# Performance work log

Measured on AMD Instinct MI355X. Metric: run time of the kernel, lower is better.

Reference implementation:

```python
import jax, jax.numpy as jnp
import numpy as np

SIGMA_INIT = 1000.0


def setup_inputs() -> dict:
    key = jax.random.key(0)
    k1, k2, k3 = jax.random.split(key, 3)
    B, M, D, S = 1024, 209, 12288, 2
    input_data = jax.random.normal(k1, (B, D), dtype=jnp.float32)
    center = jax.random.normal(k2, (M, D), dtype=jnp.float32)
    sigma = SIGMA_INIT * jnp.ones((M,), dtype=jnp.float32)
    W = 50.0 * jax.random.normal(k3, (S, M), dtype=jnp.float32)
    b = jnp.zeros((S,), dtype=jnp.float32)
    return {"input_data": input_data, "center": center, "sigma": sigma, "W": W, "b": b}


def reference(input_data, center, sigma, W, b):
    # Euclidean distance ||x_i - c_j|| via GEMM expansion (avoids [B,M,D] diff tensor)
    x2 = jnp.sum(input_data * input_data, axis=1, keepdims=True)        # [B,1]
    c2 = jnp.sum(center * center, axis=1)[None, :]                      # [1,M]
    d2 = x2 + c2 - 2.0 * (input_data @ center.T)                        # [B,M]
    dist = jnp.sqrt(jnp.maximum(d2, 0.0))
    # Note: original divides the (non-squared) norm by sigma^2, then exp(-.)
    radial = jnp.exp(-dist / (sigma * sigma)[None, :])                  # [B,M]
    return radial @ W.T + b                                             # [B,S]
```

## Files before the change

kernel.cpp:

```cpp
#include <hip/hip_runtime.h>
#include <hip/hip_bf16.h>
#include <stdint.h>

#define B_SZ 1024
#define M_SZ 209
#define MPAD 224
#define D_SZ 12288
#define KC   16
#define KCH  768
#define BK   128
#define NIT  (KCH / BK)
#define NB   32
#define BT   32
#define NCT  7
#define SROW 224
#define SLROW (KC * SROW)

#define CBF_OFF  0u
#define XXP_OFF  (MPAD * D_SZ)
#define CCP_OFF  (XXP_OFF + B_SZ * KC * 4)
#define SLAB_OFF (CCP_OFF + MPAD * 2 * 4)

typedef __attribute__((ext_vector_type(8))) short short8;
typedef __attribute__((ext_vector_type(4))) float floatx4;

__device__ __forceinline__ uint32_t pk8x4(const float4& v) {
    int d = __builtin_amdgcn_cvt_pk_fp8_f32(v.x, v.y, 0, false);
    d     = __builtin_amdgcn_cvt_pk_fp8_f32(v.z, v.w, d, true);
    return (uint32_t)d;
}

__device__ __forceinline__ void gload_lds16(const void* g, void* l) {
    __builtin_amdgcn_global_load_lds(
        (const __attribute__((address_space(1))) void*)g,
        (__attribute__((address_space(3))) void*)l, 16, 0, 0);
}

__global__ __launch_bounds__(256) void rbf_prep(
    const float* __restrict__ c, uint8_t* __restrict__ cf8,
    float* __restrict__ ccp)
{
    __shared__ float red[4];
    const int j = blockIdx.x >> 1, h = blockIdx.x & 1;
    const int t = threadIdx.x;
    const int base = h * (D_SZ / 2);
    uint8_t* dst = cf8 + (size_t)j * D_SZ + base;
    float s = 0.f;
    if (j < M_SZ) {
        const float* src = c + (size_t)j * D_SZ + base;
        for (int i = t * 8; i < D_SZ / 2; i += 2048) {
            float4 v0 = *(const float4*)(src + i);
            float4 v1 = *(const float4*)(src + i + 4);
            s += v0.x*v0.x + v0.y*v0.y + v0.z*v0.z + v0.w*v0.w
               + v1.x*v1.x + v1.y*v1.y + v1.z*v1.z + v1.w*v1.w;
            uint2 w = { pk8x4(v0), pk8x4(v1) };
            *(uint2*)(dst + i) = w;
        }
    } else {
        uint2 zz = {0u, 0u};
        for (int i = t * 8; i < D_SZ / 2; i += 2048) *(uint2*)(dst + i) = zz;
    }
#pragma unroll
    for (int off = 32; off > 0; off >>= 1) s += __shfl_down(s, off);
    if ((t & 63) == 0) red[t >> 6] = s;
    __syncthreads();
    if (t == 0) ccp[j * 2 + h] = red[0] + red[1] + red[2] + red[3];
}

__global__ __launch_bounds__(256, 2) void rbf_main(
    const float* __restrict__ x, const uint8_t* __restrict__ cf8,
    uint8_t* __restrict__ slab, float* __restrict__ xxp)
{
    __shared__ uint8_t sx[2][BT * BK];
    __shared__ uint8_t sc[2][MPAD * BK];

    const int t    = threadIdx.x;
    const int k    = blockIdx.x;
    const int b    = blockIdx.y;
    const int wave = t >> 6, lane = t & 63;
    const int quad = lane >> 4, mrow = lane & 15;
    const int qh = quad >> 1, ql = quad & 1;
    const int s2 = (mrow >> 1) & 7;
    const int rt  = wave & 1;
    const int cth = wave >> 1;

    floatx4 acc[NCT];
    const floatx4 z4 = {0.f, 0.f, 0.f, 0.f};
#pragma unroll
    for (int i = 0; i < NCT; ++i) acc[i] = z4;

    const int oE = (((lane & 7) ^ (lane >> 4)) & 7) * 16;
    const int oO = ((((lane & 7) ^ (lane >> 4)) ^ 4) & 7) * 16;
    const uint8_t* cpbE = cf8 + (size_t)(lane >> 3) * D_SZ + (size_t)k * KCH + oE;
    const uint8_t* cpbO = cf8 + (size_t)(lane >> 3) * D_SZ + (size_t)k * KCH + oO;

#pragma unroll
    for (int jj = 0; jj < 7; ++jj) {
        const int cr = wave * 7 + jj;
        const uint8_t* p = ((cr & 1) ? cpbO : cpbE) + (size_t)cr * 8 * D_SZ;
        gload_lds16(p, &sc[0][cr * 1024]);
    }

    const int xr = t >> 3;
    const int xc = t & 7;
    const float* xp = x + (size_t)(b * BT + xr) * D_SZ + (size_t)k * KCH + xc * 16;

    uint4 xw[NIT];
    float sxx = 0.f;
#pragma unroll
    for (int it = 0; it < NIT; ++it) {
        float4 v0 = *(const float4*)(xp + it * BK + 0);
        float4 v1 = *(const float4*)(xp + it * BK + 4);
        float4 v2 = *(const float4*)(xp + it * BK + 8);
        float4 v3 = *(const float4*)(xp + it * BK + 12);
        sxx += v0.x*v0.x + v0.y*v0.y + v0.z*v0.z + v0.w*v0.w
             + v1.x*v1.x + v1.y*v1.y + v1.z*v1.z + v1.w*v1.w
             + v2.x*v2.x + v2.y*v2.y + v2.z*v2.z + v2.w*v2.w
             + v3.x*v3.x + v3.y*v3.y + v3.z*v3.z + v3.w*v3.w;
        xw[it] = make_uint4(pk8x4(v0), pk8x4(v1), pk8x4(v2), pk8x4(v3));
    }
    const int sxoff = xr * BK + ((xc ^ ((xr >> 1) & 7)) & 7) * 16;

    int boff[4];
#pragma unroll
    for (int ks = 0; ks < 4; ++ks)
        boff[ks] = (((ks * 2 + qh) ^ s2) & 7) * 16 + ql * 8;
    const int aoff = (rt * 16 + mrow) * BK;
    const int boff0 = (cth * 7 * 16 + mrow) * BK;

    *(uint4*)&sx[0][sxoff] = xw[0];
    __syncthreads();

#pragma unroll
    for (int it = 0; it < NIT; ++it) {
        const int cur = it & 1;
        if (it + 1 < NIT) {
#pragma unroll
            for (int jj = 0; jj < 7; ++jj) {
                const int cr = wave * 7 + jj;
                const uint8_t* p = ((cr & 1) ? cpbO : cpbE)
                                 + (size_t)cr * 8 * D_SZ + (it + 1) * BK;
                gload_lds16(p, &sc[cur ^ 1][cr * 1024]);
            }
            *(uint4*)&sx[cur ^ 1][sxoff] = xw[it + 1];
        }
#pragma unroll
        for (int ks = 0; ks < 4; ++ks) {
            const long a = *(const long*)(&sx[cur][aoff] + boff[ks]);
#pragma unroll
            for (int ct = 0; ct < NCT; ++ct) {
                const long bv = *(const long*)(&sc[cur][boff0] + ct * 16 * BK + boff[ks]);
                acc[ct] = __builtin_amdgcn_mfma_f32_16x16x32_fp8_fp8(a, bv, acc[ct], 0, 0, 0);
            }
        }
        __syncthreads();
    }

    uint8_t* sd = slab + (size_t)k * SROW;
    const int gi0 = b * BT + rt * 16 + quad * 4;
#pragma unroll
    for (int ct = 0; ct < NCT; ++ct) {
        const int gj = (cth * 7 + ct) * 16 + mrow;
        const int p01 = __builtin_amdgcn_cvt_pk_fp8_f32(acc[ct][0], acc[ct][1], 0, false);
        const int p23 = __builtin_amdgcn_cvt_pk_fp8_f32(acc[ct][2], acc[ct][3], 0, false);
        uint8_t* wb = sd + (size_t)gi0 * SLROW + gj;
        wb[0]                   = (uint8_t)(p01 & 0xff);
        wb[SLROW]               = (uint8_t)((p01 >> 8) & 0xff);
        wb[2 * (size_t)SLROW]   = (uint8_t)(p23 & 0xff);
        wb[3 * (size_t)SLROW]   = (uint8_t)((p23 >> 8) & 0xff);
    }

    sxx += __shfl_down(sxx, 4);
    sxx += __shfl_down(sxx, 2);
    sxx += __shfl_down(sxx, 1);
    if ((t & 7) == 0) xxp[(size_t)(b * BT + xr) * KC + k] = sxx;
}

__global__ __launch_bounds__(256) void rbf_fin(
    const uint8_t* __restrict__ slab, const float* __restrict__ xxp,
    const float* __restrict__ ccp, const float* __restrict__ sigma,
    const float* __restrict__ W, const float* __restrict__ bias,
    float* __restrict__ out)
{
    __shared__ float jpart[MPAD * 9];
    __shared__ float jtot[MPAD];
    __shared__ float xsh;

    const int t = threadIdx.x;
    const int i = blockIdx.x;

    if (t < 64) {
        float xv = (t < KC) ? xxp[(size_t)i * KC + t] : 0.f;
#pragma unroll
        for (int off = 32; off > 0; off >>= 1) xv += __shfl_down(xv, off);
        if (t == 0) xsh = xv;
    }

    const int o = t % 28, g = t / 28;
    if (t < 252) {
        const uint8_t* sp = slab + (size_t)i * SLROW + o * 8;
        float s8[8] = {0.f,0.f,0.f,0.f,0.f,0.f,0.f,0.f};
        for (int kk = g; kk < KC; kk += 9) {
            uint2 v = *(const uint2*)(sp + (size_t)kk * SROW);
            s8[0] += __builtin_amdgcn_cvt_f32_fp8((int)v.x, 0);
            s8[1] += __builtin_amdgcn_cvt_f32_fp8((int)v.x, 1);
            s8[2] += __builtin_amdgcn_cvt_f32_fp8((int)v.x, 2);
            s8[3] += __builtin_amdgcn_cvt_f32_fp8((int)v.x, 3);
            s8[4] += __builtin_amdgcn_cvt_f32_fp8((int)v.y, 0);
            s8[5] += __builtin_amdgcn_cvt_f32_fp8((int)v.y, 1);
            s8[6] += __builtin_amdgcn_cvt_f32_fp8((int)v.y, 2);
            s8[7] += __builtin_amdgcn_cvt_f32_fp8((int)v.y, 3);
        }
#pragma unroll
        for (int e = 0; e < 8; ++e) jpart[(o * 8 + e) * 9 + g] = s8[e];
    }
    __syncthreads();

    if (t < MPAD) {
        float d = 0.f;
#pragma unroll
        for (int g2 = 0; g2 < 9; ++g2) d += jpart[t * 9 + g2];
        jtot[t] = d;
    }
    __syncthreads();

    if (t < 64) {
        const float xxi = xsh;
        float a0 = 0.f, a1 = 0.f;
        for (int j = t; j < M_SZ; j += 64) {
            const float ccj = ccp[j * 2] + ccp[j * 2 + 1];
            float d2 = fmaxf(xxi + ccj - 2.f * jtot[j], 0.f);
            float sg = sigma[j];
            float rad = __expf(-sqrtf(d2) / (sg * sg));
            a0 += rad * W[j];
            a1 += rad * W[M_SZ + j];
        }
#pragma unroll
        for (int off = 32; off > 0; off >>= 1) {
            a0 += __shfl_down(a0, off);
            a1 += __shfl_down(a1, off);
        }
        if (t == 0) {
            out[i * 2 + 0] = a0 + bias[0];
            out[i * 2 + 1] = a1 + bias[1];
        }
    }
}

extern "C" void kernel_launch(void* const* d_in, const int* in_sizes, int n_in,
                              void* d_out, int out_size, void* d_ws, size_t ws_size,
                              hipStream_t stream)
{
    const float* x     = (const float*)d_in[0];
    const float* c     = (const float*)d_in[1];
    const float* sigma = (const float*)d_in[2];
    const float* W     = (const float*)d_in[3];
    const float* bias  = (const float*)d_in[4];
    float* out = (float*)d_out;

    char* ws = (char*)d_ws;
    uint8_t* cf8  = (uint8_t*)(ws + CBF_OFF);
    float*   xxp  = (float*)(ws + XXP_OFF);
    float*   ccp  = (float*)(ws + CCP_OFF);
    uint8_t* slab = (uint8_t*)(ws + SLAB_OFF);

    rbf_prep<<<MPAD * 2, 256, 0, stream>>>(c, cf8, ccp);
    rbf_main<<<dim3(KC, NB), 256, 0, stream>>>(x, cf8, slab, xxp);
    rbf_fin<<<B_SZ, 256, 0, stream>>>(slab, xxp, ccp, sigma, W, bias, out);
}
```

Measured before the change: 110.5 us.

## Fuse finalize kernel into main GEMM via last-block atomic counter

Removes the separate rbf_fin launch. Each main block bumps a per-row-tile atomic counter after writing its fp8 partial slab, and the last of the KC split-K blocks does the reduction, exp and projection for its 32 rows. The counter is reset in the prep kernel. This saves a kernel launch and its gap, but puts the whole epilogue on only 32 blocks, each handling 8 rows per wave serially, which could be slower than the 1024-block finalize.

```diff
diff --git a/kernel.cpp b/kernel.cpp
--- a/kernel.cpp
+++ b/kernel.cpp
@@ -20,8 +20,8 @@
 #define XXP_OFF  (MPAD * D_SZ)
 #define CCP_OFF  (XXP_OFF + B_SZ * KC * 4)
 #define SLAB_OFF (CCP_OFF + MPAD * 2 * 4)
-
-typedef __attribute__((ext_vector_type(8))) short short8;
+#define CNT_OFF  (SLAB_OFF + B_SZ * SLROW)
+
 typedef __attribute__((ext_vector_type(4))) float floatx4;
 
 __device__ __forceinline__ uint32_t pk8x4(const float4& v) {
@@ -38,11 +38,12 @@
 
 __global__ __launch_bounds__(256) void rbf_prep(
     const float* __restrict__ c, uint8_t* __restrict__ cf8,
-    float* __restrict__ ccp)
+    float* __restrict__ ccp, uint32_t* __restrict__ cnt)
 {
     __shared__ float red[4];
     const int j = blockIdx.x >> 1, h = blockIdx.x & 1;
     const int t = threadIdx.x;
+    if (blockIdx.x == 0 && t < NB) cnt[t] = 0u;
     const int base = h * (D_SZ / 2);
     uint8_t* dst = cf8 + (size_t)j * D_SZ + base;
     float s = 0.f;
@@ -69,7 +70,10 @@
 
 __global__ __launch_bounds__(256, 2) void rbf_main(
     const float* __restrict__ x, const uint8_t* __restrict__ cf8,
-    uint8_t* __restrict__ slab, float* __restrict__ xxp)
+    uint8_t* __restrict__ slab, float* __restrict__ xxp,
+    uint32_t* __restrict__ cnt, const float* __restrict__ ccp,
+    const float* __restrict__ sigma, const float* __restrict__ W,
+    const float* __restrict__ bias, float* __restrict__ out)
 {
     __shared__ uint8_t sx[2][BT * BK];
     __shared__ uint8_t sc[2][MPAD * BK];
@@ -125,7 +129,7 @@
 #pragma unroll
     for (int ks = 0; ks < 4; ++ks)
         boff[ks] = (((ks * 2 + qh) ^ s2) & 7) * 16 + ql * 8;
-    const int aoff = (rt * 16 + mrow) * BK;
+    const int aoff  = (rt * 16 + mrow) * BK;
     const int boff0 = (cth * 7 * 16 + mrow) * BK;
 
     *(uint4*)&sx[0][sxoff] = xw[0];
@@ -156,93 +160,82 @@
         __syncthreads();
     }
 
-    uint8_t* sd = slab + (size_t)k * SROW;
-    const int gi0 = b * BT + rt * 16 + quad * 4;
-#pragma unroll
-    for (int ct = 0; ct < NCT; ++ct) {
-        const int gj = (cth * 7 + ct) * 16 + mrow;
-        const int p01 = __builtin_amdgcn_cvt_pk_fp8_f32(acc[ct][0], acc[ct][1], 0, false);
-        const int p23 = __builtin_amdgcn_cvt_pk_fp8_f32(acc[ct][2], acc[ct][3], 0, false);
-        uint8_t* wb = sd + (size_t)gi0 * SLROW + gj;
-        wb[0]                   = (uint8_t)(p01 & 0xff);
-        wb[SLROW]               = (uint8_t)((p01 >> 8) & 0xff);
-        wb[2 * (size_t)SLROW]   = (uint8_t)(p23 & 0xff);
-        wb[3 * (size_t)SLROW]   = (uint8_t)((p23 >> 8) & 0xff);
-    }
-
-    sxx += __shfl_down(sxx, 4);
-    sxx += __shfl_down(sxx, 2);
-    sxx += __shfl_down(sxx, 1);
-    if ((t & 7) == 0) xxp[(size_t)(b * BT + xr) * KC + k] = sxx;
-}
-
-__global__ __launch_bounds__(256) void rbf_fin(
-    const uint8_t* __restrict__ slab, const float* __restrict__ xxp,
-    const float* __restrict__ ccp, const float* __restrict__ sigma,
-    const float* __restrict__ W, const float* __restrict__ bias,
-    float* __restrict__ out)
-{
-    __shared__ float jpart[MPAD * 9];
-    __shared__ float jtot[MPAD];
-    __shared__ float xsh;
-
-    const int t = threadIdx.x;
-    const int i = blockIdx.x;
-
-    if (t < 64) {
-        float xv = (t < KC) ? xxp[(size_t)i * KC + t] : 0.f;
+    {
+        uint8_t* sd = slab + (size_t)k * SROW;
+        const int gi0 = b * BT + rt * 16 + quad * 4;
+#pragma unroll
+        for (int ct = 0; ct < NCT; ++ct) {
+            const int gj = (cth * 7 + ct) * 16 + mrow;
+            const int p01 = __builtin_amdgcn_cvt_pk_fp8_f32(acc[ct][0], acc[ct][1], 0, false);
+            const int p23 = __builtin_amdgcn_cvt_pk_fp8_f32(acc[ct][2], acc[ct][3], 0, false);
+            uint8_t* wb = sd + (size_t)gi0 * SLROW + gj;
+            wb[0]                 = (uint8_t)(p01 & 0xff);
+            wb[SLROW]             = (uint8_t)((p01 >> 8) & 0xff);
+            wb[2 * (size_t)SLROW] = (uint8_t)(p23 & 0xff);
+            wb[3 * (size_t)SLROW] = (uint8_t)((p23 >> 8) & 0xff);
+        }
+        sxx += __shfl_down(sxx, 4);
+        sxx += __shfl_down(sxx, 2);
+        sxx += __shfl_down(sxx, 1);
+        if ((t & 7) == 0) xxp[(size_t)(b * BT + xr) * KC + k] = sxx;
+    }
+
+    __threadfence();
+    __syncthreads();
+    int* flag = (int*)&sx[0][0];
+    if (t == 0) {
+        const uint32_t old = atomicAdd(&cnt[b], 1u);
+        *flag = (old == (uint32_t)(KC - 1)) ? 1 : 0;
+    }
+    __syncthreads();
+    if (*flag == 0) return;
+    __threadfence();
+
+    const float b0 = bias[0], b1 = bias[1];
+#pragma unroll
+    for (int r = 0; r < 8; ++r) {
+        const int i = b * BT + wave * 8 + r;
+
+        float xv = (lane < KC) ? xxp[(size_t)i * KC + lane] : 0.f;
 #pragma unroll
         for (int off = 32; off > 0; off >>= 1) xv += __shfl_down(xv, off);
-        if (t == 0) xsh = xv;
-    }
-
-    const int o = t % 28, g = t / 28;
-    if (t < 252) {
-        const uint8_t* sp = slab + (size_t)i * SLROW + o * 8;
-        float s8[8] = {0.f,0.f,0.f,0.f,0.f,0.f,0.f,0.f};
-        for (int kk = g; kk < KC; kk += 9) {
-            uint2 v = *(const uint2*)(sp + (size_t)kk * SROW);
-            s8[0] += __builtin_amdgcn_cvt_f32_fp8((int)v.x, 0);
-            s8[1] += __builtin_amdgcn_cvt_f32_fp8((int)v.x, 1);
-            s8[2] += __builtin_amdgcn_cvt_f32_fp8((int)v.x, 2);
-            s8[3] += __builtin_amdgcn_cvt_f32_fp8((int)v.x, 3);
-            s8[4] += __builtin_amdgcn_cvt_f32_fp8((int)v.y, 0);
-            s8[5] += __builtin_amdgcn_cvt_f32_fp8((int)v.y, 1);
-            s8[6] += __builtin_amdgcn_cvt_f32_fp8((int)v.y, 2);
-            s8[7] += __builtin_amdgcn_cvt_f32_fp8((int)v.y, 3);
-        }
-#pragma unroll
-        for (int e = 0; e < 8; ++e) jpart[(o * 8 + e) * 9 + g] = s8[e];
-    }
-    __syncthreads();
-
-    if (t < MPAD) {
-        float d = 0.f;
-#pragma unroll
-        for (int g2 = 0; g2 < 9; ++g2) d += jpart[t * 9 + g2];
-        jtot[t] = d;
-    }
-    __syncthreads();
-
-    if (t < 64) {
-        const float xxi = xsh;
+        const float xxi = __shfl(xv, 0);
+
+        float jt0 = 0.f, jt1 = 0.f, jt2 = 0.f, jt3 = 0.f;
+        if (lane < 56) {
+            const uint8_t* sp = slab + (size_t)i * SLROW + lane * 4;
+#pragma unroll
+            for (int kk = 0; kk < KC; ++kk) {
+                const int v = *(const int*)(sp + kk * SROW);
+                jt0 += __builtin_amdgcn_cvt_f32_fp8(v, 0);
+                jt1 += __builtin_amdgcn_cvt_f32_fp8(v, 1);
+                jt2 += __builtin_amdgcn_cvt_f32_fp8(v, 2);
+                jt3 += __builtin_amdgcn_cvt_f32_fp8(v, 3);
+            }
+        }
+
         float a0 = 0.f, a1 = 0.f;
-        for (int j = t; j < M_SZ; j += 64) {
-            const float ccj = ccp[j * 2] + ccp[j * 2 + 1];
-            float d2 = fmaxf(xxi + ccj - 2.f * jtot[j], 0.f);
-            float sg = sigma[j];
-            float rad = __expf(-sqrtf(d2) / (sg * sg));
-            a0 += rad * W[j];
-            a1 += rad * W[M_SZ + j];
+        const float jt[4] = { jt0, jt1, jt2, jt3 };
+#pragma unroll
+        for (int e = 0; e < 4; ++e) {
+            const int j = lane * 4 + e;
+            if (j < M_SZ) {
+                const float ccj = ccp[j * 2] + ccp[j * 2 + 1];
+                const float d2 = fmaxf(xxi + ccj - 2.f * jt[e], 0.f);
+                const float sg = sigma[j];
+                const float rad = __expf(-sqrtf(d2) / (sg * sg));
+                a0 += rad * W[j];
+                a1 += rad * W[M_SZ + j];
+            }
         }
 #pragma unroll
         for (int off = 32; off > 0; off >>= 1) {
             a0 += __shfl_down(a0, off);
             a1 += __shfl_down(a1, off);
         }
-        if (t == 0) {
-            out[i * 2 + 0] = a0 + bias[0];
-            out[i * 2 + 1] = a1 + bias[1];
+        if (lane == 0) {
+            out[i * 2 + 0] = a0 + b0;
+            out[i * 2 + 1] = a1 + b1;
         }
     }
 }
@@ -259,12 +252,13 @@
     float* out = (float*)d_out;
 
     char* ws = (char*)d_ws;
-    uint8_t* cf8  = (uint8_t*)(ws + CBF_OFF);
-    float*   xxp  = (float*)(ws + XXP_OFF);
-    float*   ccp  = (float*)(ws + CCP_OFF);
-    uint8_t* slab = (uint8_t*)(ws + SLAB_OFF);
-
-    rbf_prep<<<MPAD * 2, 256, 0, stream>>>(c, cf8, ccp);
-    rbf_main<<<dim3(KC, NB), 256, 0, stream>>>(x, cf8, slab, xxp);
-    rbf_fin<<<B_SZ, 256, 0, stream>>>(slab, xxp, ccp, sigma, W, bias, out);
-}
+    uint8_t*  cf8  = (uint8_t*)(ws + CBF_OFF);
+    float*    xxp  = (float*)(ws + XXP_OFF);
+    float*    ccp  = (float*)(ws + CCP_OFF);
+    uint8_t*  slab = (uint8_t*)(ws + SLAB_OFF);
+    uint32_t* cnt  = (uint32_t*)(ws + CNT_OFF);
+
+    rbf_prep<<<MPAD * 2, 256, 0, stream>>>(c, cf8, ccp, cnt);
+    rbf_main<<<dim3(KC, NB), 256, 0, stream>>>(x, cf8, slab, xxp, cnt,
+                                               ccp, sigma, W, bias, out);
+}
```

Result: slower. 191.4 us (+73.2%).
